# Optimization experiments

Measured on AMD Instinct MI355X. Metric: run time of the kernel, lower is better.

The kernel has to match this reference:

```python
import jax, jax.numpy as jnp
import numpy as np
import math

B, T, M, C, H = 2, 2048, 1024, 512, 8
D = C // H  # head dim = 64


def setup_inputs() -> dict:
    key = jax.random.key(0)
    ks = jax.random.split(key, 6)
    return {
        "x": jax.random.normal(ks[0], (B, T, C), jnp.float32),
        "y": jax.random.normal(ks[1], (B, M, C), jnp.float32),
        "attn_x_mask": jnp.ones((1, 1, T, T), jnp.int32),
        "qkv_w": jax.random.normal(ks[2], (3 * C, C), jnp.float32) * 0.02,
        "qkv_b": jax.random.normal(ks[3], (3 * C,), jnp.float32) * 0.02,
        "proj_w": jax.random.normal(ks[4], (C, C), jnp.float32) * 0.02,
        "proj_b": jax.random.normal(ks[5], (C,), jnp.float32) * 0.02,
    }


def _split_heads(t, n, d):
    # [B, N, C] -> [B, H, N, D]
    b = t.shape[0]
    return t.reshape(b, n, H, d).transpose(0, 2, 1, 3)


def reference(x, y, attn_x_mask, qkv_w, qkv_b, proj_w, proj_b):
    b, t, c = x.shape
    m = y.shape[1]
    d = c // H
    scale = 1.0 / math.sqrt(d)

    # shared qkv projection applied to x and y (torch Linear: x @ W.T + b)
    qkv_x = x @ qkv_w.T + qkv_b
    q_x, k_x, v_x = jnp.split(qkv_x, 3, axis=-1)
    qkv_y = y @ qkv_w.T + qkv_b
    q_y, k_y, v_y = jnp.split(qkv_y, 3, axis=-1)

    q_x, k_x, v_x = (_split_heads(a, t, d) for a in (q_x, k_x, v_x))
    q_y, k_y, v_y = (_split_heads(a, m, d) for a in (q_y, k_y, v_y))

    # x -> y cross attention scores (pre-softmax, reused for chaining)
    catt_x2y = jnp.einsum("bhtd,bhmd->bhtm", q_x, k_y) * scale  # [B,H,T,M]
    cval_x2y = jnp.einsum("bhtm,bhmd->bhtd", jax.nn.softmax(catt_x2y, axis=-1), v_y)
    cval_x2y = cval_x2y.transpose(0, 2, 1, 3).reshape(b, t, c)

    # y -> x scores, then chained through raw x2y scores
    catt_y2x = jnp.einsum("bhmd,bhsd->bhms", q_y, k_x) * scale  # [B,H,M,T]
    chained = jnp.einsum("bhtm,bhms->bhts", catt_x2y, catt_y2x) * scale  # [B,H,T,T]
    chained = jnp.where(attn_x_mask == 0, -jnp.inf, chained)
    cval_y2x = jnp.einsum("bhts,bhsd->bhtd", jax.nn.softmax(chained, axis=-1), v_x)
    cval_y2x = cval_y2x.transpose(0, 2, 1, 3).reshape(b, t, c)

    out = cval_x2y - cval_y2x
    out = out @ proj_w.T + proj_b  # dropout layers are identity in eval mode
    return out
```

## Files before the change

### kernel.cpp

```cpp
#include <hip/hip_runtime.h>


typedef _Float16 half_t;
typedef _Float16 half8 __attribute__((ext_vector_type(8)));
typedef _Float16 half4v __attribute__((ext_vector_type(4)));
typedef float floatx4 __attribute__((ext_vector_type(4)));
typedef int int4v __attribute__((ext_vector_type(4)));

constexpr int Bc = 2, Tc = 2048, Mc = 1024, Cc = 512, Hc = 8, Dc = 64;
constexpr long BTC = (long)Bc * Tc * Cc;
constexpr float S1 = 0.18033688f;

enum { EPI_F16STORE = 0, EPI_QKV_XY = 1, EPI_PROJ = 2 };

struct EpiParams {
  half_t* h0;
  half_t* h1;
  half_t* h2;
  half_t* h3;
  half_t* h4;
  half_t* h5;
  half_t* h6;
  float* f0;
  const float* bias;
  float scale;
  int ldc;
  long bstride;
};

__device__ __forceinline__ void gld_lds16(const half_t* g, half_t* l) {
  __builtin_amdgcn_global_load_lds(
      (const __attribute__((address_space(1))) void*)g,
      (__attribute__((address_space(3))) void*)l, 16, 0, 0);
}

__device__ __forceinline__ int pkrtz(float a, float b) {
  return __builtin_bit_cast(int, __builtin_amdgcn_cvt_pkrtz(a, b));
}
__device__ __forceinline__ void pl16(int& a, int& b) {
  asm volatile("v_permlane16_swap_b32 %0, %1" : "+v"(a), "+v"(b));
}
__device__ __forceinline__ void pl32(int& a, int& b) {
  asm volatile("v_permlane32_swap_b32 %0, %1" : "+v"(a), "+v"(b));
}

template <int BM, int BN, int WMG, int WNG, int EPI>
__global__ __launch_bounds__(256) void gemm_nt(
    const half_t* __restrict__ A, const half_t* __restrict__ Bt,
    int K, int lda, int ldb, long bsA, long bsB, EpiParams ep)
{
  constexpr int BK = 64;
  constexpr int WTM = BM / WMG, WTN = BN / WNG;
  constexpr int MI = WTM / 16, NI = WTN / 16;
  constexpr int AIT = BM * BK / 8 / 256;
  constexpr int BIT = BN * BK / 8 / 256;
  constexpr int NLD = AIT + BIT;
  __shared__ __align__(16) half_t As[2][BM * BK];
  __shared__ __align__(16) half_t Bs[2][BN * BK];

  const int tid = threadIdx.x;
  const int lane = tid & 63;
  const int wave = tid >> 6;
  const int wm = wave / WNG, wn = wave % WNG;
  const int r16 = lane & 15, g = lane >> 4;
  const int z = blockIdx.z;
  const long m0 = (long)blockIdx.y * BM;
  const long n0 = (long)blockIdx.x * BN;
  const half_t* Abase = A + (long)z * bsA + m0 * (long)lda;
  const half_t* Bbase = Bt + (long)z * bsB + n0 * (long)ldb;

  const int rA = wm * WTM + r16;
  const int rB = wn * WTN + r16;

  floatx4 acc[MI][NI];
#pragma unroll
  for (int mi = 0; mi < MI; ++mi)
#pragma unroll
    for (int ni = 0; ni < NI; ++ni)
      acc[mi][ni] = floatx4{0.f, 0.f, 0.f, 0.f};

  auto stage = [&](int kt, int buf) {
#pragma unroll
    for (int i = 0; i < AIT; ++i) {
      const int c = tid + i * 256;
      const int row = c >> 3, js = c & 7;
      const int jg = js ^ (row & 7);
      gld_lds16(Abase + (long)row * lda + kt + jg * 8, &As[buf][c * 8]);
    }
#pragma unroll
    for (int i = 0; i < BIT; ++i) {
      const int c = tid + i * 256;
      const int row = c >> 3, js = c & 7;
      const int jg = js ^ (row & 7);
      gld_lds16(Bbase + (long)row * ldb + kt + jg * 8, &Bs[buf][c * 8]);
    }
  };

  const int NIT = K / BK;
  stage(0, 0);
  asm volatile("" ::: "memory");

  for (int it = 0; it < NIT; ++it) {
    const bool hn = (it + 1 < NIT);
    if (hn) stage((it + 1) * BK, (it + 1) & 1);
    asm volatile("" ::: "memory");
    if (hn) {
      if constexpr (NLD == 6) asm volatile("s_waitcnt vmcnt(6)" ::: "memory");
      else if constexpr (NLD == 4) asm volatile("s_waitcnt vmcnt(4)" ::: "memory");
      else if constexpr (NLD == 8) asm volatile("s_waitcnt vmcnt(8)" ::: "memory");
      else asm volatile("s_waitcnt vmcnt(0)" ::: "memory");
    } else {
      asm volatile("s_waitcnt vmcnt(0)" ::: "memory");
    }
    __builtin_amdgcn_s_barrier();
    asm volatile("" ::: "memory");

    const half_t* Ab = As[it & 1];
    const half_t* Bb = Bs[it & 1];
    half8 aF[MI][2], bF[NI][2];
#pragma unroll
    for (int mi = 0; mi < MI; ++mi)
#pragma unroll
      for (int k2 = 0; k2 < 2; ++k2)
        aF[mi][k2] = *reinterpret_cast<const half8*>(
            &Ab[(rA + mi * 16) * BK + ((k2 * 4 + g) ^ (r16 & 7)) * 8]);
#pragma unroll
    for (int ni = 0; ni < NI; ++ni)
#pragma unroll
      for (int k2 = 0; k2 < 2; ++k2)
        bF[ni][k2] = *reinterpret_cast<const half8*>(
            &Bb[(rB + ni * 16) * BK + ((k2 * 4 + g) ^ (r16 & 7)) * 8]);
    __builtin_amdgcn_s_setprio(1);
#pragma unroll
    for (int k2 = 0; k2 < 2; ++k2)
#pragma unroll
      for (int mi = 0; mi < MI; ++mi)
#pragma unroll
        for (int ni = 0; ni < NI; ++ni)
          acc[mi][ni] = __builtin_amdgcn_mfma_f32_16x16x32_f16(
              aF[mi][k2], bF[ni][k2], acc[mi][ni], 0, 0, 0);
    __builtin_amdgcn_s_setprio(0);
    asm volatile("s_waitcnt lgkmcnt(0)" ::: "memory");
    __builtin_amdgcn_s_barrier();
    asm volatile("" ::: "memory");
  }

#pragma unroll
  for (int mi = 0; mi < MI; ++mi) {
#pragma unroll
    for (int ni = 0; ni < NI; ++ni) {
#pragma unroll
      for (int reg = 0; reg < 4; ++reg) {
        const int r = (int)m0 + wm * WTM + mi * 16 + g * 4 + reg;
        const int c = (int)n0 + wn * WTN + ni * 16 + r16;
        const float v = acc[mi][ni][reg];
        if constexpr (EPI == EPI_F16STORE) {
          ep.h0[(long)z * ep.bstride + (long)r * ep.ldc + c] = (half_t)(v * ep.scale);
        } else if constexpr (EPI == EPI_QKV_XY) {
          const float val = v + ep.bias[c];
          const int which = c >> 9;
          const int cc2 = c & 511;
          const int h = cc2 >> 6, d = cc2 & 63;
          if (r < Bc * Tc) {
            const int b = r >> 11, t = r & (Tc - 1);
            const long bh = (long)(b * Hc + h);
            if (which == 0)      ep.h0[(bh * Tc + t) * Dc + d] = (half_t)(val * S1);
            else if (which == 1) ep.h1[(bh * Tc + t) * Dc + d] = (half_t)val;
            else                 ep.h2[(bh * Dc + d) * Tc + t] = (half_t)val;
          } else {
            const int r2 = r - Bc * Tc;
            const int b = r2 >> 10, t = r2 & (Mc - 1);
            const long bh = (long)(b * Hc + h);
            if (which == 0)      ep.h3[(bh * Dc + d) * Mc + t] = (half_t)(val * 0.125f);
            else if (which == 1) { ep.h4[(bh * Mc + t) * Dc + d] = (half_t)val;
                                   ep.h5[(bh * Dc + d) * Mc + t] = (half_t)val; }
            else                 ep.h6[(bh * Dc + d) * Mc + t] = (half_t)val;
          }
        } else {
          ep.f0[(long)r * Cc + c] = v + ep.bias[c];
        }
      }
    }
  }
}

__global__ __launch_bounds__(256) void wtq2(
    const half_t* __restrict__ QYT, const half_t* __restrict__ KYT,
    const half_t* __restrict__ QX, half_t* __restrict__ Q2)
{
  __shared__ __align__(16) half_t As[2][4096];
  __shared__ __align__(16) half_t Bs[2][4096];
  __shared__ __align__(16) half_t WTs[4096];
  const int tid = threadIdx.x, lane = tid & 63, wave = tid >> 6;
  const int wm = wave >> 1, wn = wave & 1;
  const int r16 = lane & 15, g = lane >> 4;
  const int z = blockIdx.y;
  const int t0 = blockIdx.x * 128;
  const half_t* Aq = QYT + (long)z * Dc * Mc;
  const half_t* Bk = KYT + (long)z * Dc * Mc;

  auto stage1 = [&](int kt, int buf) {
#pragma unroll
    for (int i = 0; i < 2; ++i) {
      const int c = tid + i * 256;
      const int row = c >> 3, js = c & 7, jg = js ^ (row & 7);
      gld_lds16(Aq + (long)row * Mc + kt + jg * 8, &As[buf][c * 8]);
    }
#pragma unroll
    for (int i = 0; i < 2; ++i) {
      const int c = tid + i * 256;
      const int row = c >> 3, js = c & 7, jg = js ^ (row & 7);
      gld_lds16(Bk + (long)row * Mc + kt + jg * 8, &Bs[buf][c * 8]);
    }
  };

  floatx4 acc[2][2];
#pragma unroll
  for (int mi = 0; mi < 2; ++mi)
#pragma unroll
    for (int ni = 0; ni < 2; ++ni) acc[mi][ni] = floatx4{0.f, 0.f, 0.f, 0.f};

  const int rA = wm * 32 + r16, rB = wn * 32 + r16;
  stage1(0, 0);
  asm volatile("" ::: "memory");
  for (int it = 0; it < 16; ++it) {
    const bool hn = (it < 15);
    if (hn) stage1((it + 1) * 64, (it + 1) & 1);
    asm volatile("" ::: "memory");
    if (hn) asm volatile("s_waitcnt vmcnt(4)" ::: "memory");
    else    asm volatile("s_waitcnt vmcnt(0)" ::: "memory");
    __builtin_amdgcn_s_barrier();
    asm volatile("" ::: "memory");
    const half_t* Ab = As[it & 1];
    const half_t* Bb = Bs[it & 1];
    half8 aF[2][2], bF[2][2];
#pragma unroll
    for (int mi = 0; mi < 2; ++mi)
#pragma unroll
      for (int k2 = 0; k2 < 2; ++k2)
        aF[mi][k2] = *reinterpret_cast<const half8*>(
            &Ab[(rA + mi * 16) * 64 + ((k2 * 4 + g) ^ (r16 & 7)) * 8]);
#pragma unroll
    for (int ni = 0; ni < 2; ++ni)
#pragma unroll
      for (int k2 = 0; k2 < 2; ++k2)
        bF[ni][k2] = *reinterpret_cast<const half8*>(
            &Bb[(rB + ni * 16) * 64 + ((k2 * 4 + g) ^ (r16 & 7)) * 8]);
    __builtin_amdgcn_s_setprio(1);
#pragma unroll
    for (int k2 = 0; k2 < 2; ++k2)
#pragma unroll
      for (int mi = 0; mi < 2; ++mi)
#pragma unroll
        for (int ni = 0; ni < 2; ++ni)
          acc[mi][ni] = __builtin_amdgcn_mfma_f32_16x16x32_f16(
              aF[mi][k2], bF[ni][k2], acc[mi][ni], 0, 0, 0);
    __builtin_amdgcn_s_setprio(0);
    asm volatile("s_waitcnt lgkmcnt(0)" ::: "memory");
    __builtin_amdgcn_s_barrier();
    asm volatile("" ::: "memory");
  }

  half_t* P2 = &As[0][0];
#pragma unroll
  for (int i = 0; i < 4; ++i) {
    const int c = tid + i * 256;
    const int row = c >> 3, js = c & 7, jg = js ^ (row & 7);
    gld_lds16(QX + ((long)z * Tc + t0 + row) * 64 + jg * 8, P2 + c * 8);
  }
#pragma unroll
  for (int mi = 0; mi < 2; ++mi)
#pragma unroll
    for (int ni = 0; ni < 2; ++ni)
#pragma unroll
      for (int reg = 0; reg < 4; ++reg) {
        const int r = wm * 32 + mi * 16 + g * 4 + reg;
        const int c = wn * 32 + ni * 16 + r16;
        WTs[r * 64 + (((c >> 3) ^ (r & 7)) << 3) + (c & 7)] =
            (half_t)(acc[mi][ni][reg] * 0.125f);
      }
  __syncthreads();

  floatx4 a2[2][4];
#pragma unroll
  for (int mi = 0; mi < 2; ++mi)
#pragma unroll
    for (int ni = 0; ni < 4; ++ni) a2[mi][ni] = floatx4{0.f, 0.f, 0.f, 0.f};
  const int rA2 = wave * 32 + r16;
  half8 aF2[2][2], bF2[4][2];
#pragma unroll
  for (int mi = 0; mi < 2; ++mi)
#pragma unroll
    for (int k2 = 0; k2 < 2; ++k2)
      aF2[mi][k2] = *reinterpret_cast<const half8*>(
          &P2[(rA2 + mi * 16) * 64 + ((k2 * 4 + g) ^ (r16 & 7)) * 8]);
#pragma unroll
  for (int ni = 0; ni < 4; ++ni)
#pragma unroll
    for (int k2 = 0; k2 < 2; ++k2)
      bF2[ni][k2] = *reinterpret_cast<const half8*>(
          &WTs[(ni * 16 + r16) * 64 + ((k2 * 4 + g) ^ (r16 & 7)) * 8]);
#pragma unroll
  for (int k2 = 0; k2 < 2; ++k2)
#pragma unroll
    for (int mi = 0; mi < 2; ++mi)
#pragma unroll
      for (int ni = 0; ni < 4; ++ni)
        a2[mi][ni] = __builtin_amdgcn_mfma_f32_16x16x32_f16(
            aF2[mi][k2], bF2[ni][k2], a2[mi][ni], 0, 0, 0);
#pragma unroll
  for (int mi = 0; mi < 2; ++mi)
#pragma unroll
    for (int ni = 0; ni < 4; ++ni)
#pragma unroll
      for (int reg = 0; reg < 4; ++reg) {
        const int t = t0 + wave * 32 + mi * 16 + g * 4 + reg;
        const int c = ni * 16 + r16;
        Q2[((long)z * Tc + t) * 64 + c] = (half_t)a2[mi][ni][reg];
      }
}

__device__ __forceinline__ void stageK128(const half_t* Kz, int s0, half_t* dst, int tid) {
#pragma unroll
  for (int i = 0; i < 4; ++i) {
    const int c = tid + i * 256;
    const int row = c >> 3, js = c & 7;
    const int jg = js ^ (row & 7);
    gld_lds16(Kz + (long)(s0 + row) * 64 + jg * 8, dst + c * 8);
  }
}
__device__ __forceinline__ void stageV128(const half_t* Vz, int s0, int Slen, half_t* dst, int tid) {
#pragma unroll
  for (int i = 0; i < 4; ++i) {
    const int c = tid + i * 256;
    const int row = c >> 4, js = c & 15;
    const int jg = js ^ (row & 15);
    gld_lds16(Vz + (long)row * Slen + s0 + jg * 8, dst + c * 8);
  }
}

template <bool MASKED, bool F32OUT>
__device__ __forceinline__ void flash_body(
    const half_t* __restrict__ Qp, const half_t* __restrict__ Kp,
    const half_t* __restrict__ Vp, const unsigned char* __restrict__ mpk,
    float* __restrict__ PO, half_t* __restrict__ outF,
    int Slen, int scount, int z, int q0,
    half_t* Kb0, half_t* Kb1, half_t* Vb0, half_t* Vb1)
{
  const int tid = threadIdx.x, lane = tid & 63, w = tid >> 6;
  const int r16 = lane & 15, g = lane >> 4;
  const int b = z >> 3, h = z & 7;
  const int NT = Slen >> 7;
  const half_t* Qz = Qp + ((long)z * Tc + q0) * 64;
  const half_t* Kz = Kp + (long)z * Slen * 64;
  const half_t* Vz = Vp + (long)z * 64 * Slen;

  stageK128(Kz, 0, Kb0, tid);
  stageV128(Vz, 0, Slen, Vb0, tid);
  asm volatile("" ::: "memory");

  half8 aQ[2][2];
#pragma unroll
  for (int mi = 0; mi < 2; ++mi)
#pragma unroll
    for (int k2 = 0; k2 < 2; ++k2)
      aQ[mi][k2] = *reinterpret_cast<const half8*>(
          Qz + (w * 32 + mi * 16 + r16) * 64 + k2 * 32 + g * 8);

  floatx4 oaccT[2][4];
  float lsum[2];
#pragma unroll
  for (int mi = 0; mi < 2; ++mi) {
    lsum[mi] = 0.f;
#pragma unroll
    for (int no = 0; no < 4; ++no) oaccT[mi][no] = floatx4{0.f, 0.f, 0.f, 0.f};
  }

  const int nt = scount >> 7;
  for (int t = 0; t < nt; ++t) {
    const bool hn = (t + 1 < nt);
    const int s0 = t << 7;
    asm volatile("s_waitcnt vmcnt(0)" ::: "memory");
    __builtin_amdgcn_s_barrier();
    asm volatile("" ::: "memory");
    if (hn) {
      stageK128(Kz, s0 + 128, (t & 1) ? Kb0 : Kb1, tid);
      stageV128(Vz, s0 + 128, Slen, (t & 1) ? Vb0 : Vb1, tid);
    }
    asm volatile("" ::: "memory");

    unsigned int mb32[2];
    if constexpr (MASKED) {
#pragma unroll
      for (int mi = 0; mi < 2; ++mi) {
        const int q = q0 + w * 32 + mi * 16 + r16;
        mb32[mi] = *reinterpret_cast<const unsigned int*>(
            mpk + ((long)q * NT + t) * 16 + 4 * g);
      }
    }

    floatx4 sacc[2][8];
#pragma unroll
    for (int mi = 0; mi < 2; ++mi)
#pragma unroll
      for (int ni = 0; ni < 8; ++ni) sacc[mi][ni] = floatx4{0.f, 0.f, 0.f, 0.f};
    const half_t* Kc = (t & 1) ? Kb1 : Kb0;
    const half_t* Vc = (t & 1) ? Vb1 : Vb0;
    __builtin_amdgcn_s_setprio(1);
#pragma unroll
    for (int ni = 0; ni < 8; ++ni) {
      const int rB = ni * 16 + r16;
      const half8 b0 = *reinterpret_cast<const half8*>(&Kc[rB * 64 + (g ^ (rB & 7)) * 8]);
      const half8 b1 = *reinterpret_cast<const half8*>(&Kc[rB * 64 + ((4 + g) ^ (rB & 7)) * 8]);
#pragma unroll
      for (int mi = 0; mi < 2; ++mi) {
        sacc[mi][ni] = __builtin_amdgcn_mfma_f32_16x16x32_f16(b0, aQ[mi][0], sacc[mi][ni], 0, 0, 0);
        sacc[mi][ni] = __builtin_amdgcn_mfma_f32_16x16x32_f16(b1, aQ[mi][1], sacc[mi][ni], 0, 0, 0);
      }
    }
    __builtin_amdgcn_s_setprio(0);

#pragma unroll
    for (int c = 0; c < 4; ++c) {
#pragma unroll
      for (int mi = 0; mi < 2; ++mi) {
#pragma unroll
        for (int hf = 0; hf < 2; ++hf) {
          const int ni = 2 * c + hf;
          if constexpr (MASKED) {
            if (mb32[mi] != 0xffffffffu) {
#pragma unroll
              for (int reg = 0; reg < 4; ++reg)
                if (!((mb32[mi] >> (reg * 8 + ni)) & 1)) sacc[mi][ni][reg] = -__builtin_inff();
            }
          }
#pragma unroll
          for (int reg = 0; reg < 4; ++reg) {
            const float e = __builtin_amdgcn_exp2f(sacc[mi][ni][reg]);
            sacc[mi][ni][reg] = e;
            lsum[mi] += e;
          }
        }
      }
      half8 bVv[4];
#pragma unroll
      for (int no = 0; no < 4; ++no) {
        const int rV = no * 16 + r16;
        bVv[no] = *reinterpret_cast<const half8*>(
            &Vc[rV * 128 + ((c * 4 + g) ^ (rV & 15)) * 8]);
      }
#pragma unroll
      for (int mi = 0; mi < 2; ++mi) {
        int x0 = pkrtz(sacc[mi][2 * c][0],     sacc[mi][2 * c][1]);
        int x1 = pkrtz(sacc[mi][2 * c][2],     sacc[mi][2 * c][3]);
        int x2 = pkrtz(sacc[mi][2 * c + 1][0], sacc[mi][2 * c + 1][1]);
        int x3 = pkrtz(sacc[mi][2 * c + 1][2], sacc[mi][2 * c + 1][3]);
        pl32(x0, x2); pl32(x1, x3);
        pl16(x0, x2); pl16(x1, x3);
        int4v wv; wv[0] = x0; wv[1] = x1; wv[2] = x2; wv[3] = x3;
        const half8 aP = __builtin_bit_cast(half8, wv);
        __builtin_amdgcn_s_setprio(1);
#pragma unroll
        for (int no = 0; no < 4; ++no)
          oaccT[mi][no] = __builtin_amdgcn_mfma_f32_16x16x32_f16(bVv[no], aP, oaccT[mi][no], 0, 0, 0);
        __builtin_amdgcn_s_setprio(0);
      }
    }
  }

  float lr[2];
#pragma unroll
  for (int mi = 0; mi < 2; ++mi) {
    float ls = lsum[mi];
    ls += __shfl_xor(ls, 16);
    ls += __shfl_xor(ls, 32);
    lr[mi] = 1.f / ls;
  }
  float* slab = reinterpret_cast<float*>(Vb0) + w * 1024;
#pragma unroll
  for (int mi = 0; mi < 2; ++mi) {
    const int tq = q0 + w * 32 + mi * 16;
#pragma unroll
    for (int no = 0; no < 4; ++no) {
      floatx4 v = oaccT[mi][no] * lr[mi];
      *reinterpret_cast<floatx4*>(&slab[r16 * 64 + no * 16 + (g ^ (r16 & 3)) * 4]) = v;
    }
#pragma unroll
    for (int it = 0; it < 4; ++it) {
      const int q2 = it * 4 + g;
      const int d4 = r16;
      const floatx4 v = *reinterpret_cast<const floatx4*>(
          &slab[q2 * 64 + (d4 >> 2) * 16 + ((d4 & 3) ^ (q2 & 3)) * 4]);
      const long off = ((long)(b * Tc + tq + q2)) * Cc + h * 64 + d4 * 4;
      if constexpr (F32OUT) {
        *reinterpret_cast<floatx4*>(&PO[off]) = v;
      } else {
        half4v hh; hh[0] = (half_t)v[0]; hh[1] = (half_t)v[1];
        hh[2] = (half_t)v[2]; hh[3] = (half_t)v[3];
        *reinterpret_cast<half4v*>(&outF[off]) = hh;
      }
    }
  }
}

__global__ __launch_bounds__(256, 2) void flash_both(
    const half_t* __restrict__ Q2, const half_t* __restrict__ KX,
    const half_t* __restrict__ VXT, const unsigned char* __restrict__ mpk,
    const half_t* __restrict__ QX, const half_t* __restrict__ KY,
    const half_t* __restrict__ VYT,
    float* __restrict__ PO, half_t* __restrict__ DH2)
{
  __shared__ __align__(16) half_t Kb0[8192];
  __shared__ __align__(16) half_t Kb1[8192];
  __shared__ __align__(16) half_t Vb0[8192];
  __shared__ __align__(16) half_t Vb1[8192];
  const int bx = blockIdx.x;
  if (bx < 256) {
    const int z  = ((bx & 7) << 1) | ((bx >> 3) & 1);
    const int q0 = (bx >> 4) * 128;
    flash_body<true, true>(Q2, KX, VXT, mpk, PO, nullptr,
                           Tc, Tc, z, q0, Kb0, Kb1, Vb0, Vb1);
  } else {
    const int b2 = bx - 256;
    const int z  = ((b2 & 7) << 1) | ((b2 >> 3) & 1);
    const int q0 = (b2 >> 4) * 128;
    flash_body<false, false>(QX, KY, VYT, nullptr, nullptr, DH2,
                             Mc, Mc, z, q0, Kb0, Kb1, Vb0, Vb1);
  }
}

__global__ __launch_bounds__(256) void gemm_proj(
    const half_t* __restrict__ DH2, const float* __restrict__ PO,
    const half_t* __restrict__ WP, const float* __restrict__ bias,
    float* __restrict__ out)
{
  constexpr int BK = 64, NIT = 8;
  __shared__ __align__(16) half_t As[2][64 * 64];
  __shared__ __align__(16) half_t Bs[2][64 * 64];
  const int tid = threadIdx.x, lane = tid & 63, wave = tid >> 6;
  const int wm = wave >> 1, wn = wave & 1;
  const int r16 = lane & 15, g = lane >> 4;
  const long m0 = (long)blockIdx.y * 64;
  const long n0 = (long)blockIdx.x * 64;

  half8  a_d2[2][2];
  float4 a_po[2][2][2];

  auto issueA = [&](int kt, int buf) {
#pragma unroll
    for (int i = 0; i < 2; ++i) {
      const int c = tid + i * 256;
      const int row = c >> 3, js = c & 7, jg = js ^ (row & 7);
      const long off = (m0 + row) * Cc + kt + jg * 8;
      a_d2[buf][i] = *reinterpret_cast<const half8*>(&DH2[off]);
      a_po[buf][i][0] = *reinterpret_cast<const float4*>(&PO[off]);
      a_po[buf][i][1] = *reinterpret_cast<const float4*>(&PO[off + 4]);
    }
  };
  auto issueB = [&](int kt, int buf) {
#pragma unroll
    for (int i = 0; i < 2; ++i) {
      const int c = tid + i * 256;
      const int row = c >> 3, js = c & 7, jg = js ^ (row & 7);
      gld_lds16(WP + (n0 + row) * Cc + kt + jg * 8, &Bs[buf][c * 8]);
    }
  };

  floatx4 acc[2][2];
#pragma unroll
  for (int mi = 0; mi < 2; ++mi)
#pragma unroll
    for (int ni = 0; ni < 2; ++ni) acc[mi][ni] = floatx4{0.f, 0.f, 0.f, 0.f};

  const int rA = wm * 32 + r16, rB = wn * 32 + r16;

  issueA(0, 0); issueB(0, 0);
  asm volatile("" ::: "memory");

#pragma unroll
  for (int t = 0; t < NIT; ++t) {
    const bool hn = (t + 1 < NIT);
    if (hn) { issueA((t + 1) * BK, (t + 1) & 1); issueB((t + 1) * BK, (t + 1) & 1); }
    asm volatile("" ::: "memory");
    if (hn) asm volatile("s_waitcnt vmcnt(8)" ::: "memory");
    else    asm volatile("s_waitcnt vmcnt(0)" ::: "memory");
#pragma unroll
    for (int i = 0; i < 2; ++i) {
      const int c = tid + i * 256;
      const float4 p0 = a_po[t & 1][i][0], p1 = a_po[t & 1][i][1];
      const half8 d2 = a_d2[t & 1][i];
      int w0 = pkrtz((float)d2[0] - p0.x, (float)d2[1] - p0.y);
      int w1 = pkrtz((float)d2[2] - p0.z, (float)d2[3] - p0.w);
      int w2 = pkrtz((float)d2[4] - p1.x, (float)d2[5] - p1.y);
      int w3 = pkrtz((float)d2[6] - p1.z, (float)d2[7] - p1.w);
      int4v wv; wv[0] = w0; wv[1] = w1; wv[2] = w2; wv[3] = w3;
      *reinterpret_cast<int4v*>(&As[t & 1][c * 8]) = wv;
    }
    asm volatile("s_waitcnt lgkmcnt(0)" ::: "memory");
    __builtin_amdgcn_s_barrier();
    asm volatile("" ::: "memory");

    half8 aF[2][2], bF[2][2];
#pragma unroll
    for (int mi = 0; mi < 2; ++mi)
#pragma unroll
      for (int k2 = 0; k2 < 2; ++k2)
        aF[mi][k2] = *reinterpret_cast<const half8*>(
            &As[t & 1][(rA + mi * 16) * BK + ((k2 * 4 + g) ^ (r16 & 7)) * 8]);
#pragma unroll
    for (int ni = 0; ni < 2; ++ni)
#pragma unroll
      for (int k2 = 0; k2 < 2; ++k2)
        bF[ni][k2] = *reinterpret_cast<const half8*>(
            &Bs[t & 1][(rB + ni * 16) * BK + ((k2 * 4 + g) ^ (r16 & 7)) * 8]);
    __builtin_amdgcn_s_setprio(1);
#pragma unroll
    for (int k2 = 0; k2 < 2; ++k2)
#pragma unroll
      for (int mi = 0; mi < 2; ++mi)
#pragma unroll
        for (int ni = 0; ni < 2; ++ni)
          acc[mi][ni] = __builtin_amdgcn_mfma_f32_16x16x32_f16(
              aF[mi][k2], bF[ni][k2], acc[mi][ni], 0, 0, 0);
    __builtin_amdgcn_s_setprio(0);
    asm volatile("s_waitcnt lgkmcnt(0)" ::: "memory");
    __builtin_amdgcn_s_barrier();
    asm volatile("" ::: "memory");
  }

#pragma unroll
  for (int mi = 0; mi < 2; ++mi)
#pragma unroll
    for (int ni = 0; ni < 2; ++ni)
#pragma unroll
      for (int reg = 0; reg < 4; ++reg) {
        const long r = m0 + wm * 32 + mi * 16 + g * 4 + reg;
        const int  c = (int)n0 + wn * 32 + ni * 16 + r16;
        out[r * Cc + c] = acc[mi][ni][reg] + bias[c];
      }
}

__device__ __forceinline__ void cvt4(const float* in, half_t* out, long i) {
  const float4 f = reinterpret_cast<const float4*>(in)[i];
  half4v h; h[0] = (half_t)f.x; h[1] = (half_t)f.y; h[2] = (half_t)f.z; h[3] = (half_t)f.w;
  reinterpret_cast<half4v*>(out)[i] = h;
}

__global__ __launch_bounds__(256) void prep(
    const float* __restrict__ x, const float* __restrict__ y,
    const float* __restrict__ qw, const float* __restrict__ pw,
    const int* __restrict__ mask,
    half_t* __restrict__ XH, half_t* __restrict__ YH,
    half_t* __restrict__ WQ, half_t* __restrict__ WP,
    unsigned char* __restrict__ mpk)
{
  const long i = (long)blockIdx.x * 256 + threadIdx.x;
  constexpr long n0 = 524288;
  constexpr long n1 = n0 + 262144;
  constexpr long n2 = n1 + 196608;
  constexpr long n3 = n2 + 65536;
  if (i < n0) cvt4(x, XH, i);
  else if (i < n1) cvt4(y, YH, i - n0);
  else if (i < n2) cvt4(qw, WQ, i - n1);
  else if (i < n3) cvt4(pw, WP, i - n2);
  else {
    const long idx = i - n3;
    const int t = (int)(idx >> 8), tile = (int)((idx >> 4) & 15), r16 = (int)(idx & 15);
    const int* row = mask + (long)t * Tc + tile * 128 + r16;
    unsigned int bbits = 0;
#pragma unroll
    for (int ni = 0; ni < 8; ++ni)
      bbits |= (row[ni * 16] != 0 ? 1u : 0u) << ni;
    mpk[idx] = (unsigned char)bbits;
  }
}

constexpr size_t OFF_XH   = 0;
constexpr size_t OFF_YH   = OFF_XH   + (size_t)Bc*Tc*Cc*2;
constexpr size_t OFF_WQ   = OFF_YH   + (size_t)Bc*Mc*Cc*2;
constexpr size_t OFF_WP   = OFF_WQ   + (size_t)3*Cc*Cc*2;
constexpr size_t OFF_QX   = OFF_WP   + (size_t)Cc*Cc*2;
constexpr size_t OFF_KX   = OFF_QX   + (size_t)Bc*Hc*Tc*Dc*2;
constexpr size_t OFF_VXT  = OFF_KX   + (size_t)Bc*Hc*Tc*Dc*2;
constexpr size_t OFF_QYT  = OFF_VXT  + (size_t)Bc*Hc*Tc*Dc*2;
constexpr size_t OFF_KY   = OFF_QYT  + (size_t)Bc*Hc*Mc*Dc*2;
constexpr size_t OFF_KYT  = OFF_KY   + (size_t)Bc*Hc*Mc*Dc*2;
constexpr size_t OFF_VYT  = OFF_KYT  + (size_t)Bc*Hc*Mc*Dc*2;
constexpr size_t OFF_Q2   = OFF_VYT  + (size_t)Bc*Hc*Mc*Dc*2;
constexpr size_t OFF_DH2  = OFF_Q2   + (size_t)Bc*Hc*Tc*Dc*2;
constexpr size_t OFF_MPK  = OFF_DH2  + (size_t)Bc*Tc*Cc*2;
constexpr size_t OFF_PO   = OFF_MPK  + (size_t)Tc*256;

extern "C" void kernel_launch(void* const* d_in, const int* in_sizes, int n_in,
                              void* d_out, int out_size, void* d_ws, size_t ws_size,
                              hipStream_t stream) {
  const float* x      = (const float*)d_in[0];
  const float* y      = (const float*)d_in[1];
  const int*   mask   = (const int*)  d_in[2];
  const float* qkv_b  = (const float*)d_in[4];
  const float* proj_b = (const float*)d_in[6];
  float* out = (float*)d_out;
  char* ws = (char*)d_ws;

  half_t* XH   = (half_t*)(ws + OFF_XH);
  half_t* YH   = (half_t*)(ws + OFF_YH);
  half_t* WQ   = (half_t*)(ws + OFF_WQ);
  half_t* WP   = (half_t*)(ws + OFF_WP);
  half_t* QX   = (half_t*)(ws + OFF_QX);
  half_t* KX   = (half_t*)(ws + OFF_KX);
  half_t* VXT  = (half_t*)(ws + OFF_VXT);
  half_t* QYT  = (half_t*)(ws + OFF_QYT);
  half_t* KY   = (half_t*)(ws + OFF_KY);
  half_t* KYT  = (half_t*)(ws + OFF_KYT);
  half_t* VYT  = (half_t*)(ws + OFF_VYT);
  half_t* Q2   = (half_t*)(ws + OFF_Q2);
  half_t* DH2  = (half_t*)(ws + OFF_DH2);
  unsigned char* MPK = (unsigned char*)(ws + OFF_MPK);
  float*  PO   = (float*) (ws + OFF_PO);

  prep<<<6144, 256, 0, stream>>>(x, y, (const float*)d_in[3], (const float*)d_in[5],
                                 mask, XH, YH, WQ, WP, MPK);

  {
    EpiParams ep{};
    ep.h0 = QX; ep.h1 = KX; ep.h2 = VXT; ep.h3 = QYT;
    ep.h4 = KY; ep.h5 = KYT; ep.h6 = VYT; ep.bias = qkv_b;
    gemm_nt<128,64,2,2,EPI_QKV_XY><<<dim3(24, 48, 1), 256, 0, stream>>>(
        XH, WQ, Cc, Cc, Cc, 0, 0, ep);
  }

  wtq2<<<dim3(16, 16), 256, 0, stream>>>(QYT, KYT, QX, Q2);

  flash_both<<<dim3(512), 256, 0, stream>>>(
      Q2, KX, VXT, MPK, QX, KY, VYT, PO, DH2);

  gemm_proj<<<dim3(8, 64), 256, 0, stream>>>(DH2, PO, WP, proj_b, out);
}
```

Before: 183.6 us.

## Split masked flash attention over key halves and combine partial sums in projection

The T×T chained attention is split into two key-range halves (split-K), which doubles its block count to 768. Each half writes unnormalised partial outputs and row sums, and the projection GEMM merges and normalises them while loading its A operand. The V tile drops to a single LDS buffer loaded inside each iteration, with the exponentials computed before a mid-iteration barrier. This cuts shared memory so launch bounds can allow 3 blocks per CU. The trade is extra fp32 partial-output traffic and less overlap for V loads, in exchange for better occupancy and load balance.

```diff
diff --git a/kernel.cpp b/kernel.cpp
--- a/kernel.cpp
+++ b/kernel.cpp
@@ -9,6 +9,7 @@
 
 constexpr int Bc = 2, Tc = 2048, Mc = 1024, Cc = 512, Hc = 8, Dc = 64;
 constexpr long BTC = (long)Bc * Tc * Cc;
+constexpr long ZT  = (long)Bc * Hc * Tc;
 constexpr float S1 = 0.18033688f;
 
 enum { EPI_F16STORE = 0, EPI_QKV_XY = 1, EPI_PROJ = 2 };
@@ -339,13 +340,13 @@
   }
 }
 
-template <bool MASKED, bool F32OUT>
+template <bool MASKED, bool PARTIAL>
 __device__ __forceinline__ void flash_body(
     const half_t* __restrict__ Qp, const half_t* __restrict__ Kp,
     const half_t* __restrict__ Vp, const unsigned char* __restrict__ mpk,
-    float* __restrict__ PO, half_t* __restrict__ outF,
-    int Slen, int scount, int z, int q0,
-    half_t* Kb0, half_t* Kb1, half_t* Vb0, half_t* Vb1)
+    float* __restrict__ PO, float* __restrict__ Lp, half_t* __restrict__ outF,
+    int Slen, int sbeg, int scount, int z, int q0,
+    half_t* Kb0, half_t* Kb1, half_t* Vb)
 {
   const int tid = threadIdx.x, lane = tid & 63, w = tid >> 6;
   const int r16 = lane & 15, g = lane >> 4;
@@ -355,8 +356,7 @@
   const half_t* Kz = Kp + (long)z * Slen * 64;
   const half_t* Vz = Vp + (long)z * 64 * Slen;
 
-  stageK128(Kz, 0, Kb0, tid);
-  stageV128(Vz, 0, Slen, Vb0, tid);
+  stageK128(Kz, sbeg, Kb0, tid);
   asm volatile("" ::: "memory");
 
   half8 aQ[2][2];
@@ -379,25 +379,23 @@
   const int nt = scount >> 7;
   for (int t = 0; t < nt; ++t) {
     const bool hn = (t + 1 < nt);
-    const int s0 = t << 7;
+    const int s0 = sbeg + (t << 7);
     asm volatile("s_waitcnt vmcnt(0)" ::: "memory");
     __builtin_amdgcn_s_barrier();
     asm volatile("" ::: "memory");
-    if (hn) {
-      stageK128(Kz, s0 + 128, (t & 1) ? Kb0 : Kb1, tid);
-      stageV128(Vz, s0 + 128, Slen, (t & 1) ? Vb0 : Vb1, tid);
-    }
-    asm volatile("" ::: "memory");
 
     unsigned int mb32[2];
     if constexpr (MASKED) {
+      const int tile = s0 >> 7;
 #pragma unroll
       for (int mi = 0; mi < 2; ++mi) {
         const int q = q0 + w * 32 + mi * 16 + r16;
         mb32[mi] = *reinterpret_cast<const unsigned int*>(
-            mpk + ((long)q * NT + t) * 16 + 4 * g);
-      }
-    }
+            mpk + ((long)q * NT + tile) * 16 + 4 * g);
+      }
+    }
+    stageV128(Vz, s0, Slen, Vb, tid);
+    asm volatile("" ::: "memory");
 
     floatx4 sacc[2][8];
 #pragma unroll
@@ -405,7 +403,6 @@
 #pragma unroll
       for (int ni = 0; ni < 8; ++ni) sacc[mi][ni] = floatx4{0.f, 0.f, 0.f, 0.f};
     const half_t* Kc = (t & 1) ? Kb1 : Kb0;
-    const half_t* Vc = (t & 1) ? Vb1 : Vb0;
     __builtin_amdgcn_s_setprio(1);
 #pragma unroll
     for (int ni = 0; ni < 8; ++ni) {
@@ -419,35 +416,45 @@
       }
     }
     __builtin_amdgcn_s_setprio(0);
+    if (hn) stageK128(Kz, s0 + 128, (t & 1) ? Kb0 : Kb1, tid);
+    asm volatile("" ::: "memory");
+
+#pragma unroll
+    for (int mi = 0; mi < 2; ++mi) {
+      if constexpr (MASKED) {
+        if (mb32[mi] != 0xffffffffu) {
+#pragma unroll
+          for (int reg = 0; reg < 4; ++reg)
+#pragma unroll
+            for (int ni = 0; ni < 8; ++ni)
+              if (!((mb32[mi] >> (reg * 8 + ni)) & 1)) sacc[mi][ni][reg] = -__builtin_inff();
+        }
+      }
+      float ls = 0.f;
+#pragma unroll
+      for (int ni = 0; ni < 8; ++ni)
+#pragma unroll
+        for (int reg = 0; reg < 4; ++reg) {
+          const float e = __builtin_amdgcn_exp2f(sacc[mi][ni][reg]);
+          sacc[mi][ni][reg] = e;
+          ls += e;
+        }
+      lsum[mi] += ls;
+    }
+
+    if (hn) { asm volatile("s_waitcnt vmcnt(4)" ::: "memory"); }
+    else    { asm volatile("s_waitcnt vmcnt(0)" ::: "memory"); }
+    __builtin_amdgcn_s_barrier();
+    asm volatile("" ::: "memory");
 
 #pragma unroll
     for (int c = 0; c < 4; ++c) {
-#pragma unroll
-      for (int mi = 0; mi < 2; ++mi) {
-#pragma unroll
-        for (int hf = 0; hf < 2; ++hf) {
-          const int ni = 2 * c + hf;
-          if constexpr (MASKED) {
-            if (mb32[mi] != 0xffffffffu) {
-#pragma unroll
-              for (int reg = 0; reg < 4; ++reg)
-                if (!((mb32[mi] >> (reg * 8 + ni)) & 1)) sacc[mi][ni][reg] = -__builtin_inff();
-            }
-          }
-#pragma unroll
-          for (int reg = 0; reg < 4; ++reg) {
-            const float e = __builtin_amdgcn_exp2f(sacc[mi][ni][reg]);
-            sacc[mi][ni][reg] = e;
-            lsum[mi] += e;
-          }
-        }
-      }
       half8 bVv[4];
 #pragma unroll
       for (int no = 0; no < 4; ++no) {
         const int rV = no * 16 + r16;
         bVv[no] = *reinterpret_cast<const half8*>(
-            &Vc[rV * 128 + ((c * 4 + g) ^ (rV & 15)) * 8]);
+            &Vb[rV * 128 + ((c * 4 + g) ^ (rV & 15)) * 8]);
       }
 #pragma unroll
       for (int mi = 0; mi < 2; ++mi) {
@@ -468,21 +475,29 @@
     }
   }
 
-  float lr[2];
+  __builtin_amdgcn_s_barrier();
+  asm volatile("" ::: "memory");
+
+  float ls2[2];
 #pragma unroll
   for (int mi = 0; mi < 2; ++mi) {
     float ls = lsum[mi];
     ls += __shfl_xor(ls, 16);
     ls += __shfl_xor(ls, 32);
-    lr[mi] = 1.f / ls;
-  }
-  float* slab = reinterpret_cast<float*>(Vb0) + w * 1024;
+    ls2[mi] = ls;
+  }
+  float* slab = reinterpret_cast<float*>(Vb) + w * 1024;
 #pragma unroll
   for (int mi = 0; mi < 2; ++mi) {
     const int tq = q0 + w * 32 + mi * 16;
+    if constexpr (PARTIAL) {
+      if (lane < 16) Lp[(long)z * Tc + tq + r16] = ls2[mi];
+    }
+    const float sc = PARTIAL ? 1.f : (1.f / ls2[mi]);
 #pragma unroll
     for (int no = 0; no < 4; ++no) {
-      floatx4 v = oaccT[mi][no] * lr[mi];
+      floatx4 v = oaccT[mi][no];
+      if constexpr (!PARTIAL) v *= sc;
       *reinterpret_cast<floatx4*>(&slab[r16 * 64 + no * 16 + (g ^ (r16 & 3)) * 4]) = v;
     }
 #pragma unroll
@@ -492,7 +507,7 @@
       const floatx4 v = *reinterpret_cast<const floatx4*>(
           &slab[q2 * 64 + (d4 >> 2) * 16 + ((d4 & 3) ^ (q2 & 3)) * 4]);
       const long off = ((long)(b * Tc + tq + q2)) * Cc + h * 64 + d4 * 4;
-      if constexpr (F32OUT) {
+      if constexpr (PARTIAL) {
         *reinterpret_cast<floatx4*>(&PO[off]) = v;
       } else {
         half4v hh; hh[0] = (half_t)v[0]; hh[1] = (half_t)v[1];
@@ -503,38 +518,40 @@
   }
 }
 
-__global__ __launch_bounds__(256, 2) void flash_both(
+__global__ __launch_bounds__(256, 3) void flash_both(
     const half_t* __restrict__ Q2, const half_t* __restrict__ KX,
     const half_t* __restrict__ VXT, const unsigned char* __restrict__ mpk,
     const half_t* __restrict__ QX, const half_t* __restrict__ KY,
     const half_t* __restrict__ VYT,
-    float* __restrict__ PO, half_t* __restrict__ DH2)
+    float* __restrict__ PO, float* __restrict__ Lp, half_t* __restrict__ DH2)
 {
   __shared__ __align__(16) half_t Kb0[8192];
   __shared__ __align__(16) half_t Kb1[8192];
-  __shared__ __align__(16) half_t Vb0[8192];
-  __shared__ __align__(16) half_t Vb1[8192];
+  __shared__ __align__(16) half_t Vb[8192];
   const int bx = blockIdx.x;
-  if (bx < 256) {
+  if (bx < 512) {
     const int z  = ((bx & 7) << 1) | ((bx >> 3) & 1);
-    const int q0 = (bx >> 4) * 128;
-    flash_body<true, true>(Q2, KX, VXT, mpk, PO, nullptr,
-                           Tc, Tc, z, q0, Kb0, Kb1, Vb0, Vb1);
+    const int sh = (bx >> 4) & 1;
+    const int q0 = (bx >> 5) * 128;
+    flash_body<true, true>(Q2, KX, VXT, mpk,
+                           PO + (long)sh * BTC, Lp + (long)sh * ZT, nullptr,
+                           Tc, sh * 1024, 1024, z, q0, Kb0, Kb1, Vb);
   } else {
-    const int b2 = bx - 256;
+    const int b2 = bx - 512;
     const int z  = ((b2 & 7) << 1) | ((b2 >> 3) & 1);
     const int q0 = (b2 >> 4) * 128;
-    flash_body<false, false>(QX, KY, VYT, nullptr, nullptr, DH2,
-                             Mc, Mc, z, q0, Kb0, Kb1, Vb0, Vb1);
+    flash_body<false, false>(QX, KY, VYT, nullptr,
+                             nullptr, nullptr, DH2,
+                             Mc, 0, Mc, z, q0, Kb0, Kb1, Vb);
   }
 }
 
 __global__ __launch_bounds__(256) void gemm_proj(
     const half_t* __restrict__ DH2, const float* __restrict__ PO,
-    const half_t* __restrict__ WP, const float* __restrict__ bias,
-    float* __restrict__ out)
+    const float* __restrict__ Lp, const half_t* __restrict__ WP,
+    const float* __restrict__ bias, float* __restrict__ out)
 {
-  constexpr int BK = 64, NIT = 8;
+  constexpr int NIT = 8;
   __shared__ __align__(16) half_t As[2][64 * 64];
   __shared__ __align__(16) half_t Bs[2][64 * 64];
   const int tid = threadIdx.x, lane = tid & 63, wave = tid >> 6;
@@ -544,25 +561,32 @@
   const long n0 = (long)blockIdx.x * 64;
 
   half8  a_d2[2][2];
-  float4 a_po[2][2][2];
-
-  auto issueA = [&](int kt, int buf) {
+  float4 a_p0[2][2][2], a_p1[2][2][2];
+  float  a_l0[2][2], a_l1[2][2];
+
+  auto issueA = [&](int t, int buf) {
 #pragma unroll
     for (int i = 0; i < 2; ++i) {
       const int c = tid + i * 256;
       const int row = c >> 3, js = c & 7, jg = js ^ (row & 7);
-      const long off = (m0 + row) * Cc + kt + jg * 8;
-      a_d2[buf][i] = *reinterpret_cast<const half8*>(&DH2[off]);
-      a_po[buf][i][0] = *reinterpret_cast<const float4*>(&PO[off]);
-      a_po[buf][i][1] = *reinterpret_cast<const float4*>(&PO[off + 4]);
+      const long r = m0 + row;
+      const long off = r * Cc + t * 64 + jg * 8;
+      a_d2[buf][i]    = *reinterpret_cast<const half8*>(&DH2[off]);
+      a_p0[buf][i][0] = *reinterpret_cast<const float4*>(&PO[off]);
+      a_p0[buf][i][1] = *reinterpret_cast<const float4*>(&PO[off + 4]);
+      a_p1[buf][i][0] = *reinterpret_cast<const float4*>(&PO[BTC + off]);
+      a_p1[buf][i][1] = *reinterpret_cast<const float4*>(&PO[BTC + off + 4]);
+      const long zt = ((r >> 11) * 8 + t) * (long)Tc + (r & (Tc - 1));
+      a_l0[buf][i] = Lp[zt];
+      a_l1[buf][i] = Lp[ZT + zt];
     }
   };
-  auto issueB = [&](int kt, int buf) {
+  auto issueB = [&](int t, int buf) {
 #pragma unroll
     for (int i = 0; i < 2; ++i) {
       const int c = tid + i * 256;
       const int row = c >> 3, js = c & 7, jg = js ^ (row & 7);
-      gld_lds16(WP + (n0 + row) * Cc + kt + jg * 8, &Bs[buf][c * 8]);
+      gld_lds16(WP + (n0 + row) * Cc + t * 64 + jg * 8, &Bs[buf][c * 8]);
     }
   };
 
@@ -580,19 +604,25 @@
 #pragma unroll
   for (int t = 0; t < NIT; ++t) {
     const bool hn = (t + 1 < NIT);
-    if (hn) { issueA((t + 1) * BK, (t + 1) & 1); issueB((t + 1) * BK, (t + 1) & 1); }
-    asm volatile("" ::: "memory");
-    if (hn) asm volatile("s_waitcnt vmcnt(8)" ::: "memory");
+    if (hn) { issueA(t + 1, (t + 1) & 1); issueB(t + 1, (t + 1) & 1); }
+    asm volatile("" ::: "memory");
+    if (hn) asm volatile("s_waitcnt vmcnt(16)" ::: "memory");
     else    asm volatile("s_waitcnt vmcnt(0)" ::: "memory");
 #pragma unroll
     for (int i = 0; i < 2; ++i) {
       const int c = tid + i * 256;
-      const float4 p0 = a_po[t & 1][i][0], p1 = a_po[t & 1][i][1];
+      const float inv = 1.f / (a_l0[t & 1][i] + a_l1[t & 1][i]);
+      const float4 p00 = a_p0[t & 1][i][0], p01 = a_p0[t & 1][i][1];
+      const float4 p10 = a_p1[t & 1][i][0], p11 = a_p1[t & 1][i][1];
       const half8 d2 = a_d2[t & 1][i];
-      int w0 = pkrtz((float)d2[0] - p0.x, (float)d2[1] - p0.y);
-      int w1 = pkrtz((float)d2[2] - p0.z, (float)d2[3] - p0.w);
-      int w2 = pkrtz((float)d2[4] - p1.x, (float)d2[5] - p1.y);
-      int w3 = pkrtz((float)d2[6] - p1.z, (float)d2[7] - p1.w);
+      int w0 = pkrtz((float)d2[0] - (p00.x + p10.x) * inv,
+                     (float)d2[1] - (p00.y + p10.y) * inv);
+      int w1 = pkrtz((float)d2[2] - (p00.z + p10.z) * inv,
+                     (float)d2[3] - (p00.w + p10.w) * inv);
+      int w2 = pkrtz((float)d2[4] - (p01.x + p11.x) * inv,
+                     (float)d2[5] - (p01.y + p11.y) * inv);
+      int w3 = pkrtz((float)d2[6] - (p01.z + p11.z) * inv,
+                     (float)d2[7] - (p01.w + p11.w) * inv);
       int4v wv; wv[0] = w0; wv[1] = w1; wv[2] = w2; wv[3] = w3;
       *reinterpret_cast<int4v*>(&As[t & 1][c * 8]) = wv;
     }
@@ -606,13 +636,13 @@
 #pragma unroll
       for (int k2 = 0; k2 < 2; ++k2)
         aF[mi][k2] = *reinterpret_cast<const half8*>(
-            &As[t & 1][(rA + mi * 16) * BK + ((k2 * 4 + g) ^ (r16 & 7)) * 8]);
+            &As[t & 1][(rA + mi * 16) * 64 + ((k2 * 4 + g) ^ (r16 & 7)) * 8]);
 #pragma unroll
     for (int ni = 0; ni < 2; ++ni)
 #pragma unroll
       for (int k2 = 0; k2 < 2; ++k2)
         bF[ni][k2] = *reinterpret_cast<const half8*>(
-            &Bs[t & 1][(rB + ni * 16) * BK + ((k2 * 4 + g) ^ (r16 & 7)) * 8]);
+            &Bs[t & 1][(rB + ni * 16) * 64 + ((k2 * 4 + g) ^ (r16 & 7)) * 8]);
     __builtin_amdgcn_s_setprio(1);
 #pragma unroll
     for (int k2 = 0; k2 < 2; ++k2)
@@ -690,6 +720,7 @@
 constexpr size_t OFF_DH2  = OFF_Q2   + (size_t)Bc*Hc*Tc*Dc*2;
 constexpr size_t OFF_MPK  = OFF_DH2  + (size_t)Bc*Tc*Cc*2;
 constexpr size_t OFF_PO   = OFF_MPK  + (size_t)Tc*256;
+constexpr size_t OFF_L    = OFF_PO   + (size_t)2*BTC*4;
 
 extern "C" void kernel_launch(void* const* d_in, const int* in_sizes, int n_in,
                               void* d_out, int out_size, void* d_ws, size_t ws_size,
@@ -717,6 +748,7 @@
   half_t* DH2  = (half_t*)(ws + OFF_DH2);
   unsigned char* MPK = (unsigned char*)(ws + OFF_MPK);
   float*  PO   = (float*) (ws + OFF_PO);
+  float*  Lp   = (float*) (ws + OFF_L);
 
   prep<<<6144, 256, 0, stream>>>(x, y, (const float*)d_in[3], (const float*)d_in[5],
                                  mask, XH, YH, WQ, WP, MPK);
@@ -731,8 +763,8 @@
 
   wtq2<<<dim3(16, 16), 256, 0, stream>>>(QYT, KYT, QX, Q2);
 
-  flash_both<<<dim3(512), 256, 0, stream>>>(
-      Q2, KX, VXT, MPK, QX, KY, VYT, PO, DH2);
-
-  gemm_proj<<<dim3(8, 64), 256, 0, stream>>>(DH2, PO, WP, proj_b, out);
-}
+  flash_both<<<dim3(768), 256, 0, stream>>>(
+      Q2, KX, VXT, MPK, QX, KY, VYT, PO, Lp, DH2);
+
+  gemm_proj<<<dim3(8, 64), 256, 0, stream>>>(DH2, PO, Lp, WP, proj_b, out);
+}
```

New measurement: 194.3 us. +5.9%, slower.
